# Kernel tuning notes

Measured on AMD Instinct MI355X. Metric: run time of the kernel, lower is better.

The kernel has to match this reference:

```python
import jax, jax.numpy as jnp
import numpy as np

NEG_INF = -jnp.inf


def setup_inputs() -> dict:
    key = jax.random.key(0)
    ks = jax.random.split(key, 8)
    B, C, H, W = 8, 512, 96, 96
    IC = max(1, C // 8)  # inter_channels = 64
    s = 1.0 / np.sqrt(C)
    x = jax.random.normal(ks[0], (B, C, H, W), dtype=jnp.float32)
    Wq = jax.random.normal(ks[1], (IC, C), dtype=jnp.float32) * s
    bq = jax.random.normal(ks[2], (IC,), dtype=jnp.float32) * s
    Wk = jax.random.normal(ks[3], (IC, C), dtype=jnp.float32) * s
    bk = jax.random.normal(ks[4], (IC,), dtype=jnp.float32) * s
    Wv = jax.random.normal(ks[5], (C, C), dtype=jnp.float32) * s
    bv = jax.random.normal(ks[6], (C,), dtype=jnp.float32) * s
    gamma = jnp.full((1,), 0.5, dtype=jnp.float32)  # nn.Parameter (zeros in torch; nonzero here for a non-trivial baseline)
    return {"x": x, "Wq": Wq, "bq": bq, "Wk": Wk, "bk": bk, "Wv": Wv, "bv": bv, "gamma": gamma}


def reference(x, Wq, bq, Wk, bk, Wv, bv, gamma):
    B, C, H, W = x.shape
    # 1x1 convs as channel contractions
    q = jnp.einsum('oc,bchw->bohw', Wq, x) + bq[None, :, None, None]
    k = jnp.einsum('oc,bchw->bohw', Wk, x) + bk[None, :, None, None]
    v = jnp.einsum('oc,bchw->bohw', Wv, x) + bv[None, :, None, None]
    # column (height-axis) attention logits: [B, H, W, H'] with -inf on h==h'
    e_h = jnp.einsum('bchw,bcgw->bhwg', q, k)
    eye = jnp.eye(H, dtype=bool)[:, None, :]  # [H,1,H'] broadcast over W
    e_h = jnp.where(eye[None], NEG_INF, e_h)
    # row (width-axis) attention logits: [B, H, W, W']
    e_w = jnp.einsum('bchw,bchv->bhwv', q, k)
    # joint softmax over concatenated H'+W' axis
    attn = jax.nn.softmax(jnp.concatenate([e_h, e_w], axis=-1), axis=-1)
    a_h = attn[..., :H]   # [B,H,W,H']
    a_w = attn[..., H:]   # [B,H,W,W']
    out_h = jnp.einsum('bcgw,bhwg->bchw', v, a_h)
    out_w = jnp.einsum('bchv,bhwv->bchw', v, a_w)
    return gamma[0] * (out_h + out_w) + x
```

## Files before the change

### kernel.cpp

```cpp
#include <hip/hip_runtime.h>
#include <hip/hip_bf16.h>

typedef __hip_bfloat16 bf16;
typedef unsigned short us8 __attribute__((ext_vector_type(8)));
typedef __attribute__((ext_vector_type(8))) short short8v;
typedef __attribute__((ext_vector_type(4))) float float4v;

__device__ __forceinline__ float us2f(unsigned short u){
  return __uint_as_float(((unsigned int)u) << 16);
}
__device__ __forceinline__ float b2f(bf16 v){ return __bfloat162float(v); }
__device__ __forceinline__ bf16 f2b(float v){ return __float2bfloat16(v); }
__device__ __forceinline__ unsigned short f2bu(float v){
  bf16 t = f2b(v); return *reinterpret_cast<unsigned short*>(&t);
}

#define HW 9216
#define CH 512
#define NQ 640

__global__ void k_detect(const unsigned int* __restrict__ xw, int* __restrict__ flag){
  int t = threadIdx.x;
  int cnt = 0;
  for(int i=t;i<4096;i+=256){
    unsigned e = (xw[i]>>8)&0x7F;
    if(e==0x3E||e==0x3F) cnt++;
  }
  #pragma unroll
  for(int o=32;o>0;o>>=1) cnt += __shfl_xor(cnt,o);
  __shared__ int s[4];
  if((t&63)==0) s[t>>6]=cnt;
  __syncthreads();
  if(t==0){ int tot=s[0]+s[1]+s[2]+s[3]; *flag = (tot > 1228) ? 1 : 0; }
}

__global__ void k_pack(const void* __restrict__ Wq, const void* __restrict__ Wk,
                       const void* __restrict__ Wv, const void* __restrict__ bq,
                       const void* __restrict__ bk, const void* __restrict__ bv,
                       const int* __restrict__ flag,
                       bf16* __restrict__ Wall, float* __restrict__ ball){
  bool isbf = (*flag)!=0;
  int j = blockIdx.x, t = threadIdx.x;
  const void* src = (j < 64) ? Wq : (j < 128) ? Wk : Wv;
  int row = (j < 64) ? j : (j < 128) ? (j-64) : (j-128);
  for(int c=t;c<512;c+=256){
    float v = isbf ? b2f(((const bf16*)src)[(size_t)row*512+c])
                   : ((const float*)src)[(size_t)row*512+c];
    Wall[(size_t)j*512+c] = f2b(v);
  }
  if(t==0){
    const void* bsrc = (j<64)? bq : (j<128)? bk : bv;
    ball[j] = isbf ? b2f(((const bf16*)bsrc)[row]) : ((const float*)bsrc)[row];
  }
}

__global__ __launch_bounds__(256) void k_xcvt(const void* __restrict__ x,
    const int* __restrict__ flag, bf16* __restrict__ xT){
  __shared__ float T[64][65];
  bool isbf = (*flag)!=0;
  int b = blockIdx.z, c0 = blockIdx.y*64, hw0 = blockIdx.x*64;
  int tid = threadIdx.x;
  if(isbf){
    const bf16* xb = (const bf16*)x + ((size_t)b*CH + c0)*HW + hw0;
    #pragma unroll
    for(int i=0;i<2;i++){
      int e = i*256 + tid;
      int cc = e>>3, h8 = (e&7)*8;
      us8 v = *(const us8*)(xb + (size_t)cc*HW + h8);
      #pragma unroll
      for(int j=0;j<8;j++) T[cc][h8+j] = us2f(v[j]);
    }
  } else {
    const float* xb = (const float*)x + ((size_t)b*CH + c0)*HW + hw0;
    #pragma unroll
    for(int i=0;i<4;i++){
      int e = i*256 + tid;
      int cc = e>>4, h4 = (e&15)*4;
      float4 v = *(const float4*)(xb + (size_t)cc*HW + h4);
      T[cc][h4]=v.x; T[cc][h4+1]=v.y; T[cc][h4+2]=v.z; T[cc][h4+3]=v.w;
    }
  }
  __syncthreads();
  bf16* tb = xT + ((size_t)b*HW + hw0)*512 + c0;
  #pragma unroll
  for(int i=0;i<2;i++){
    int e = i*256 + tid;
    int r = e>>3, c8 = (e&7)*8;
    us8 o;
    #pragma unroll
    for(int j=0;j<8;j++) o[j] = f2bu(T[c8+j][r]);
    *(us8*)(tb + (size_t)r*512 + c8) = o;
  }
}

__global__ __launch_bounds__(256) void k_qkv(const bf16* __restrict__ xT,
    const bf16* __restrict__ Wall, const float* __restrict__ ball,
    bf16* __restrict__ Ot){
  __shared__ ushort As[128][72];
  __shared__ ushort Bs[128][72];
  int b = blockIdx.y;
  int bx = blockIdx.x;
  int swz = (bx & 7)*45 + (bx >> 3);
  int m0 = (swz/5)*128;
  int n0 = (swz%5)*128;
  int tid = threadIdx.x, wid = tid>>6, lane = tid&63;
  int m0w = (wid>>1)*64, n0w = (wid&1)*64;
  const bf16* Ab = xT + ((size_t)b*HW + m0)*512;
  const bf16* Bb = Wall + (size_t)n0*512;
  float4v acc[4][4];
  #pragma unroll
  for(int mt=0;mt<4;mt++)
    #pragma unroll
    for(int nt=0;nt<4;nt++) acc[mt][nt] = (float4v){0.f,0.f,0.f,0.f};
  for(int k0=0;k0<512;k0+=64){
    #pragma unroll
    for(int i=0;i<4;i++){
      int s = tid + i*256;
      int row = s>>3, ko = (s&7)*8;
      us8 v = *(const us8*)(Ab + (size_t)row*512 + k0 + ko);
      *(us8*)&As[row][ko] = v;
      us8 w = *(const us8*)(Bb + (size_t)row*512 + k0 + ko);
      *(us8*)&Bs[row][ko] = w;
    }
    __syncthreads();
    #pragma unroll
    for(int kk=0;kk<64;kk+=32){
      short8v a[4], bb[4];
      #pragma unroll
      for(int mt=0;mt<4;mt++) a[mt] = *(short8v*)&As[m0w+mt*16+(lane&15)][kk+8*(lane>>4)];
      #pragma unroll
      for(int nt=0;nt<4;nt++) bb[nt] = *(short8v*)&Bs[n0w+nt*16+(lane&15)][kk+8*(lane>>4)];
      #pragma unroll
      for(int mt=0;mt<4;mt++)
        #pragma unroll
        for(int nt=0;nt<4;nt++)
          acc[mt][nt] = __builtin_amdgcn_mfma_f32_16x16x32_bf16(a[mt], bb[nt], acc[mt][nt], 0,0,0);
    }
    __syncthreads();
  }
  #pragma unroll
  for(int mt=0;mt<4;mt++){
    #pragma unroll
    for(int nt=0;nt<4;nt++){
      int nn = n0 + n0w + nt*16 + (lane&15);
      float bias = ball[nn];
      int mbase = m0 + m0w + mt*16 + (lane>>4)*4;
      #pragma unroll
      for(int r=0;r<4;r++)
        Ot[((size_t)b*HW + mbase + r)*640 + nn] = f2b(acc[mt][nt][r] + bias);
    }
  }
}

__global__ __launch_bounds__(384) void k_eh(const bf16* __restrict__ Ot,
                                            float* __restrict__ eh2){
  __shared__ ushort Qs[96][72];
  __shared__ ushort Ks[96][72];
  int b = blockIdx.y, w = blockIdx.x;
  int tid = threadIdx.x, wid = tid>>6, lane = tid&63;
  const bf16* qb = Ot + ((size_t)b*HW + w)*640;
  #pragma unroll
  for(int i=0;i<2;i++){
    int e = tid + i*384;
    int row = e>>3, ko = (e&7)*8;
    us8 q = *(const us8*)(qb + (size_t)row*96*640 + ko);
    *(us8*)&Qs[row][ko] = q;
    us8 k = *(const us8*)(qb + (size_t)row*96*640 + 64 + ko);
    *(us8*)&Ks[row][ko] = k;
  }
  __syncthreads();
  float4v acc[6];
  #pragma unroll
  for(int nt=0;nt<6;nt++) acc[nt] = (float4v){0.f,0.f,0.f,0.f};
  #pragma unroll
  for(int kt=0;kt<2;kt++){
    int kb = kt*32 + 8*(lane>>4);
    short8v a = *(short8v*)&Qs[wid*16 + (lane&15)][kb];
    #pragma unroll
    for(int nt=0;nt<6;nt++){
      short8v bb = *(short8v*)&Ks[nt*16 + (lane&15)][kb];
      acc[nt] = __builtin_amdgcn_mfma_f32_16x16x32_bf16(a, bb, acc[nt], 0,0,0);
    }
  }
  int hbase = wid*16 + (lane>>4)*4;
  #pragma unroll
  for(int nt=0;nt<6;nt++){
    int g = nt*16 + (lane&15);
    #pragma unroll
    for(int r=0;r<4;r++){
      int h = hbase + r;
      eh2[((size_t)b*HW + (size_t)h*96 + w)*96 + g] =
          (g==h) ? -INFINITY : acc[nt][r];
    }
  }
}

__global__ __launch_bounds__(384) void k_ewsm(const bf16* __restrict__ Ot,
    const float* __restrict__ eh2, bf16* __restrict__ att){
  __shared__ char smem[38400];
  ushort (*Qs)[72] = (ushort(*)[72])smem;
  ushort (*Ks)[72] = (ushort(*)[72])(smem + 13824);
  float  (*Ew)[100] = (float(*)[100])smem;
  int b = blockIdx.y, h = blockIdx.x;
  int tid = threadIdx.x, wid = tid>>6, lane = tid&63;
  const bf16* qb = Ot + ((size_t)b*HW + (size_t)h*96)*640;
  #pragma unroll
  for(int i=0;i<2;i++){
    int e = tid + i*384;
    int row = e>>3, ko = (e&7)*8;
    us8 q = *(const us8*)(qb + (size_t)row*640 + ko);
    *(us8*)&Qs[row][ko] = q;
    us8 k = *(const us8*)(qb + (size_t)row*640 + 64 + ko);
    *(us8*)&Ks[row][ko] = k;
  }
  __syncthreads();
  float4v acc[6];
  #pragma unroll
  for(int nt=0;nt<6;nt++) acc[nt] = (float4v){0.f,0.f,0.f,0.f};
  #pragma unroll
  for(int kt=0;kt<2;kt++){
    int kb = kt*32 + 8*(lane>>4);
    short8v a = *(short8v*)&Qs[wid*16 + (lane&15)][kb];
    #pragma unroll
    for(int nt=0;nt<6;nt++){
      short8v bb = *(short8v*)&Ks[nt*16 + (lane&15)][kb];
      acc[nt] = __builtin_amdgcn_mfma_f32_16x16x32_bf16(a, bb, acc[nt], 0,0,0);
    }
  }
  __syncthreads();
  int wbase = wid*16 + (lane>>4)*4;
  #pragma unroll
  for(int nt=0;nt<6;nt++){
    int v = nt*16 + (lane&15);
    #pragma unroll
    for(int r=0;r<4;r++) Ew[wbase+r][v] = acc[nt][r];
  }
  __syncthreads();
  const float* ehb = eh2 + ((size_t)b*HW + (size_t)h*96)*96;
  bf16* ab = att + ((size_t)b*HW + (size_t)h*96)*192;
  for(int r=0;r<16;r++){
    int w = wid*16 + r;
    const float* er = ehb + (size_t)w*96;
    float v0 = er[lane];
    float v1 = (lane<32) ? er[64+lane] : Ew[w][lane-32];
    float v2 = Ew[w][lane+32];
    float m = fmaxf(fmaxf(v0,v1),v2);
    #pragma unroll
    for(int o=32;o>0;o>>=1) m = fmaxf(m, __shfl_xor(m,o));
    v0=__expf(v0-m); v1=__expf(v1-m); v2=__expf(v2-m);
    float s = v0+v1+v2;
    #pragma unroll
    for(int o=32;o>0;o>>=1) s += __shfl_xor(s,o);
    float inv = 1.0f/s;
    bf16* a = ab + (size_t)w*192;
    a[lane]=f2b(v0*inv); a[lane+64]=f2b(v1*inv); a[lane+128]=f2b(v2*inv);
  }
}

__global__ __launch_bounds__(384) void k_outw(const bf16* __restrict__ Ot,
    const bf16* __restrict__ att, bf16* __restrict__ P){
  __shared__ ushort As[96][104];
  __shared__ ushort Bs[128][104];
  int b = blockIdx.y;
  int h = blockIdx.x >> 2, c0 = (blockIdx.x & 3)*128;
  int tid = threadIdx.x, wid = tid>>6, lane = tid&63;
  const bf16* ab = att + ((size_t)b*HW + (size_t)h*96)*192 + 96;
  #pragma unroll
  for(int i=0;i<3;i++){
    int s = tid + i*384;
    int row = s/12, ko = (s%12)*8;
    us8 v = *(const us8*)(ab + (size_t)row*192 + ko);
    *(us8*)&As[row][ko] = v;
  }
  const bf16* vb = Ot + ((size_t)b*HW + (size_t)h*96)*640 + 128 + c0;
  #pragma unroll
  for(int i=0;i<4;i++){
    int s = tid + i*384;
    int g = s % 96, cc = s / 96;
    us8 v = *(const us8*)(vb + (size_t)g*640 + cc*8);
    #pragma unroll
    for(int j=0;j<8;j++) Bs[cc*8+j][g] = v[j];
  }
  __syncthreads();
  float4v acc[8];
  #pragma unroll
  for(int nt=0;nt<8;nt++) acc[nt] = (float4v){0.f,0.f,0.f,0.f};
  #pragma unroll
  for(int kt=0;kt<3;kt++){
    int kb = kt*32 + 8*(lane>>4);
    short8v a = *(short8v*)&As[wid*16 + (lane&15)][kb];
    #pragma unroll
    for(int nt=0;nt<8;nt++){
      short8v bb = *(short8v*)&Bs[nt*16 + (lane&15)][kb];
      acc[nt] = __builtin_amdgcn_mfma_f32_16x16x32_bf16(a, bb, acc[nt], 0,0,0);
    }
  }
  bf16* Pb = P + ((size_t)b*HW + (size_t)h*96)*512 + c0;
  int mb = wid*16 + (lane>>4)*4;
  #pragma unroll
  for(int nt=0;nt<8;nt++){
    int n = nt*16 + (lane&15);
    #pragma unroll
    for(int r=0;r<4;r++)
      Pb[(size_t)(mb + r)*512 + n] = f2b(acc[nt][r]);
  }
}

__global__ __launch_bounds__(384) void k_outh(const bf16* __restrict__ Ot,
    const bf16* __restrict__ att, bf16* __restrict__ P){
  __shared__ ushort As[96][104];
  __shared__ ushort Bs[128][104];
  int b = blockIdx.y;
  int w = blockIdx.x >> 2, c0 = (blockIdx.x & 3)*128;
  int tid = threadIdx.x, wid = tid>>6, lane = tid&63;
  const bf16* ab = att + ((size_t)b*HW + w)*192;
  #pragma unroll
  for(int i=0;i<3;i++){
    int s = tid + i*384;
    int row = s/12, ko = (s%12)*8;
    us8 v = *(const us8*)(ab + (size_t)row*96*192 + ko);
    *(us8*)&As[row][ko] = v;
  }
  const bf16* vb = Ot + ((size_t)b*HW + w)*640 + 128 + c0;
  #pragma unroll
  for(int i=0;i<4;i++){
    int s = tid + i*384;
    int g = s % 96, cc = s / 96;
    us8 v = *(const us8*)(vb + (size_t)g*96*640 + cc*8);
    #pragma unroll
    for(int j=0;j<8;j++) Bs[cc*8+j][g] = v[j];
  }
  __syncthreads();
  float4v acc[8];
  #pragma unroll
  for(int nt=0;nt<8;nt++) acc[nt] = (float4v){0.f,0.f,0.f,0.f};
  #pragma unroll
  for(int kt=0;kt<3;kt++){
    int kb = kt*32 + 8*(lane>>4);
    short8v a = *(short8v*)&As[wid*16 + (lane&15)][kb];
    #pragma unroll
    for(int nt=0;nt<8;nt++){
      short8v bb = *(short8v*)&Bs[nt*16 + (lane&15)][kb];
      acc[nt] = __builtin_amdgcn_mfma_f32_16x16x32_bf16(a, bb, acc[nt], 0,0,0);
    }
  }
  bf16* Pb = P + ((size_t)b*HW + w)*512 + c0;
  int mb = wid*16 + (lane>>4)*4;
  #pragma unroll
  for(int nt=0;nt<8;nt++){
    int n = nt*16 + (lane&15);
    #pragma unroll
    for(int r=0;r<4;r++){
      size_t o = (size_t)(mb + r)*96*512 + n;
      Pb[o] = f2b(b2f(Pb[o]) + acc[nt][r]);
    }
  }
}

__global__ __launch_bounds__(256) void k_final(const bf16* __restrict__ P,
    const void* __restrict__ x, const void* __restrict__ gamma,
    const int* __restrict__ flag, void* __restrict__ out){
  __shared__ float T[64][65];
  bool isbf = (*flag)!=0;
  int b = blockIdx.z; int hw0 = blockIdx.x*64; int c0 = blockIdx.y*64;
  int tid = threadIdx.x;
  float g = isbf ? b2f(((const bf16*)gamma)[0]) : ((const float*)gamma)[0];
  const bf16* Pb = P + ((size_t)b*HW + hw0)*CH + c0;
  #pragma unroll
  for(int i=0;i<2;i++){
    int e = i*256 + tid;
    int r = e>>3, c8 = (e&7)*8;
    us8 v = *(const us8*)(Pb + (size_t)r*CH + c8);
    #pragma unroll
    for(int j=0;j<8;j++) T[c8+j][r] = us2f(v[j]);
  }
  __syncthreads();
  if(isbf){
    const bf16* xb = (const bf16*)x + ((size_t)b*CH + c0)*HW + hw0;
    bf16* ob = (bf16*)out + ((size_t)b*CH + c0)*HW + hw0;
    #pragma unroll
    for(int i=0;i<2;i++){
      int e = i*256 + tid;
      int cc = e>>3, h8 = (e&7)*8;
      us8 xv = *(const us8*)(xb + (size_t)cc*HW + h8);
      us8 o;
      #pragma unroll
      for(int j=0;j<8;j++) o[j] = f2bu(g*T[cc][h8+j] + us2f(xv[j]));
      *(us8*)(ob + (size_t)cc*HW + h8) = o;
    }
  } else {
    const float* xb = (const float*)x + ((size_t)b*CH + c0)*HW + hw0;
    float* ob = (float*)out + ((size_t)b*CH + c0)*HW + hw0;
    #pragma unroll
    for(int i=0;i<4;i++){
      int e = i*256 + tid;
      int cc = e>>4, h4 = (e&15)*4;
      float4 xv = *(const float4*)(xb + (size_t)cc*HW + h4);
      float4 o;
      o.x = g*T[cc][h4]   + xv.x;
      o.y = g*T[cc][h4+1] + xv.y;
      o.z = g*T[cc][h4+2] + xv.z;
      o.w = g*T[cc][h4+3] + xv.w;
      *(float4*)(ob + (size_t)cc*HW + h4) = o;
    }
  }
}

extern "C" void kernel_launch(void* const* d_in, const int* in_sizes, int n_in,
                              void* d_out, int out_size, void* d_ws, size_t ws_size,
                              hipStream_t stream){
  (void)in_sizes; (void)n_in; (void)out_size; (void)ws_size;
  const void* x     = d_in[0];
  const void* Wq    = d_in[1];
  const void* bq    = d_in[2];
  const void* Wk    = d_in[3];
  const void* bk    = d_in[4];
  const void* Wv    = d_in[5];
  const void* bv    = d_in[6];
  const void* gamma = d_in[7];
  char* ws = (char*)d_ws;

  bf16*  Wall = (bf16*)(ws + 0);
  float* ball = (float*)(ws + 655360);
  int*   flag = (int*)(ws + 657920);
  bf16*  Ot   = (bf16*)(ws + (1u<<20));
  bf16*  att  = (bf16*)(ws + 95420416ull);
  bf16*  xT   = (bf16*)(ws + 123731968ull);
  float* eh2  = (float*)(ws + 123731968ull);
  bf16*  P    = (bf16*)(ws + 123731968ull);

  hipLaunchKernelGGL(k_detect, dim3(1),       dim3(256), 0, stream,
                     (const unsigned int*)x, flag);
  hipLaunchKernelGGL(k_pack,   dim3(640),     dim3(256), 0, stream,
                     Wq, Wk, Wv, bq, bk, bv, flag, Wall, ball);
  hipLaunchKernelGGL(k_xcvt,   dim3(144,8,8), dim3(256), 0, stream, x, flag, xT);
  hipLaunchKernelGGL(k_qkv,    dim3(360,8),   dim3(256), 0, stream, xT, Wall, ball, Ot);
  hipLaunchKernelGGL(k_eh,     dim3(96,8),    dim3(384), 0, stream, Ot, eh2);
  hipLaunchKernelGGL(k_ewsm,   dim3(96,8),    dim3(384), 0, stream, Ot, eh2, att);
  hipLaunchKernelGGL(k_outw,   dim3(384,8),   dim3(384), 0, stream, Ot, att, P);
  hipLaunchKernelGGL(k_outh,   dim3(384,8),   dim3(384), 0, stream, Ot, att, P);
  hipLaunchKernelGGL(k_final,  dim3(144,8,8), dim3(256), 0, stream, P, x, gamma, flag, d_out);
}
```

Before: 311.5 us.

## Fuse width-attention output with residual epilogue and drop separate final kernel

Reorders the output stage: k_outh now writes its partial directly to P without a read-modify-write. A new k_outwf computes the width-axis attention output, adds the P partial, scales by gamma and adds x, writing the final NCHW output. It transposes the MFMA roles so each wave owns channel rows, which lets stores go straight to channel-major output. This removes one full read and write pass of P and one kernel launch. The cost is stores that are strided by HW across channels with only 16 contiguous elements per wave row, plus a fused kernel that is heavier in registers and shared memory.

```diff
diff --git a/kernel.cpp b/kernel.cpp
--- a/kernel.cpp
+++ b/kernel.cpp
@@ -257,55 +257,6 @@
   }
 }
 
-__global__ __launch_bounds__(384) void k_outw(const bf16* __restrict__ Ot,
-    const bf16* __restrict__ att, bf16* __restrict__ P){
-  __shared__ ushort As[96][104];
-  __shared__ ushort Bs[128][104];
-  int b = blockIdx.y;
-  int h = blockIdx.x >> 2, c0 = (blockIdx.x & 3)*128;
-  int tid = threadIdx.x, wid = tid>>6, lane = tid&63;
-  const bf16* ab = att + ((size_t)b*HW + (size_t)h*96)*192 + 96;
-  #pragma unroll
-  for(int i=0;i<3;i++){
-    int s = tid + i*384;
-    int row = s/12, ko = (s%12)*8;
-    us8 v = *(const us8*)(ab + (size_t)row*192 + ko);
-    *(us8*)&As[row][ko] = v;
-  }
-  const bf16* vb = Ot + ((size_t)b*HW + (size_t)h*96)*640 + 128 + c0;
-  #pragma unroll
-  for(int i=0;i<4;i++){
-    int s = tid + i*384;
-    int g = s % 96, cc = s / 96;
-    us8 v = *(const us8*)(vb + (size_t)g*640 + cc*8);
-    #pragma unroll
-    for(int j=0;j<8;j++) Bs[cc*8+j][g] = v[j];
-  }
-  __syncthreads();
-  float4v acc[8];
-  #pragma unroll
-  for(int nt=0;nt<8;nt++) acc[nt] = (float4v){0.f,0.f,0.f,0.f};
-  #pragma unroll
-  for(int kt=0;kt<3;kt++){
-    int kb = kt*32 + 8*(lane>>4);
-    short8v a = *(short8v*)&As[wid*16 + (lane&15)][kb];
-    #pragma unroll
-    for(int nt=0;nt<8;nt++){
-      short8v bb = *(short8v*)&Bs[nt*16 + (lane&15)][kb];
-      acc[nt] = __builtin_amdgcn_mfma_f32_16x16x32_bf16(a, bb, acc[nt], 0,0,0);
-    }
-  }
-  bf16* Pb = P + ((size_t)b*HW + (size_t)h*96)*512 + c0;
-  int mb = wid*16 + (lane>>4)*4;
-  #pragma unroll
-  for(int nt=0;nt<8;nt++){
-    int n = nt*16 + (lane&15);
-    #pragma unroll
-    for(int r=0;r<4;r++)
-      Pb[(size_t)(mb + r)*512 + n] = f2b(acc[nt][r]);
-  }
-}
-
 __global__ __launch_bounds__(384) void k_outh(const bf16* __restrict__ Ot,
     const bf16* __restrict__ att, bf16* __restrict__ P){
   __shared__ ushort As[96][104];
@@ -352,56 +303,71 @@
     #pragma unroll
     for(int r=0;r<4;r++){
       size_t o = (size_t)(mb + r)*96*512 + n;
-      Pb[o] = f2b(b2f(Pb[o]) + acc[nt][r]);
-    }
-  }
-}
-
-__global__ __launch_bounds__(256) void k_final(const bf16* __restrict__ P,
+      Pb[o] = f2b(acc[nt][r]);
+    }
+  }
+}
+
+__global__ __launch_bounds__(512) void k_outwf(const bf16* __restrict__ Ot,
+    const bf16* __restrict__ att, const bf16* __restrict__ P,
     const void* __restrict__ x, const void* __restrict__ gamma,
     const int* __restrict__ flag, void* __restrict__ out){
-  __shared__ float T[64][65];
+  __shared__ ushort As[96][104];
+  __shared__ ushort Bs[128][104];
   bool isbf = (*flag)!=0;
-  int b = blockIdx.z; int hw0 = blockIdx.x*64; int c0 = blockIdx.y*64;
-  int tid = threadIdx.x;
+  int b = blockIdx.y;
+  int h = blockIdx.x >> 2, c0 = (blockIdx.x & 3)*128;
+  int tid = threadIdx.x, wid = tid>>6, lane = tid&63;
   float g = isbf ? b2f(((const bf16*)gamma)[0]) : ((const float*)gamma)[0];
-  const bf16* Pb = P + ((size_t)b*HW + hw0)*CH + c0;
-  #pragma unroll
-  for(int i=0;i<2;i++){
-    int e = i*256 + tid;
-    int r = e>>3, c8 = (e&7)*8;
-    us8 v = *(const us8*)(Pb + (size_t)r*CH + c8);
-    #pragma unroll
-    for(int j=0;j<8;j++) T[c8+j][r] = us2f(v[j]);
-  }
-  __syncthreads();
-  if(isbf){
-    const bf16* xb = (const bf16*)x + ((size_t)b*CH + c0)*HW + hw0;
-    bf16* ob = (bf16*)out + ((size_t)b*CH + c0)*HW + hw0;
-    #pragma unroll
-    for(int i=0;i<2;i++){
-      int e = i*256 + tid;
-      int cc = e>>3, h8 = (e&7)*8;
-      us8 xv = *(const us8*)(xb + (size_t)cc*HW + h8);
-      us8 o;
-      #pragma unroll
-      for(int j=0;j<8;j++) o[j] = f2bu(g*T[cc][h8+j] + us2f(xv[j]));
-      *(us8*)(ob + (size_t)cc*HW + h8) = o;
-    }
-  } else {
-    const float* xb = (const float*)x + ((size_t)b*CH + c0)*HW + hw0;
-    float* ob = (float*)out + ((size_t)b*CH + c0)*HW + hw0;
-    #pragma unroll
-    for(int i=0;i<4;i++){
-      int e = i*256 + tid;
-      int cc = e>>4, h4 = (e&15)*4;
-      float4 xv = *(const float4*)(xb + (size_t)cc*HW + h4);
-      float4 o;
-      o.x = g*T[cc][h4]   + xv.x;
-      o.y = g*T[cc][h4+1] + xv.y;
-      o.z = g*T[cc][h4+2] + xv.z;
-      o.w = g*T[cc][h4+3] + xv.w;
-      *(float4*)(ob + (size_t)cc*HW + h4) = o;
+  const bf16* ab = att + ((size_t)b*HW + (size_t)h*96)*192 + 96;
+  #pragma unroll
+  for(int i=0;i<3;i++){
+    int s = tid + i*512;
+    if(s < 1152){
+      int row = s/12, ko = (s%12)*8;
+      us8 v = *(const us8*)(ab + (size_t)row*192 + ko);
+      *(us8*)&As[row][ko] = v;
+    }
+  }
+  const bf16* vb = Ot + ((size_t)b*HW + (size_t)h*96)*640 + 128 + c0;
+  #pragma unroll
+  for(int i=0;i<3;i++){
+    int s = tid + i*512;
+    int gg = s % 96, cc = s / 96;
+    us8 v = *(const us8*)(vb + (size_t)gg*640 + cc*8);
+    #pragma unroll
+    for(int j=0;j<8;j++) Bs[cc*8+j][gg] = v[j];
+  }
+  __syncthreads();
+  float4v acc[6];
+  #pragma unroll
+  for(int nt=0;nt<6;nt++) acc[nt] = (float4v){0.f,0.f,0.f,0.f};
+  #pragma unroll
+  for(int kt=0;kt<3;kt++){
+    int kb = kt*32 + 8*(lane>>4);
+    short8v a = *(short8v*)&Bs[wid*16 + (lane&15)][kb];
+    #pragma unroll
+    for(int nt=0;nt<6;nt++){
+      short8v bb = *(short8v*)&As[nt*16 + (lane&15)][kb];
+      acc[nt] = __builtin_amdgcn_mfma_f32_16x16x32_bf16(a, bb, acc[nt], 0,0,0);
+    }
+  }
+  int clb = wid*16 + (lane>>4)*4;
+  const bf16* Pb = P + ((size_t)b*HW + (size_t)h*96)*512 + c0;
+  size_t xbase = ((size_t)b*CH + c0)*HW + (size_t)h*96;
+  #pragma unroll
+  for(int nt=0;nt<6;nt++){
+    int w = nt*16 + (lane&15);
+    #pragma unroll
+    for(int r=0;r<4;r++){
+      int c = clb + r;
+      float sum = acc[nt][r] + b2f(Pb[(size_t)w*512 + c]);
+      size_t o = xbase + (size_t)c*HW + w;
+      if(isbf){
+        ((bf16*)out)[o] = f2b(g*sum + b2f(((const bf16*)x)[o]));
+      } else {
+        ((float*)out)[o] = g*sum + ((const float*)x)[o];
+      }
     }
   }
 }
@@ -437,7 +403,7 @@
   hipLaunchKernelGGL(k_qkv,    dim3(360,8),   dim3(256), 0, stream, xT, Wall, ball, Ot);
   hipLaunchKernelGGL(k_eh,     dim3(96,8),    dim3(384), 0, stream, Ot, eh2);
   hipLaunchKernelGGL(k_ewsm,   dim3(96,8),    dim3(384), 0, stream, Ot, eh2, att);
-  hipLaunchKernelGGL(k_outw,   dim3(384,8),   dim3(384), 0, stream, Ot, att, P);
   hipLaunchKernelGGL(k_outh,   dim3(384,8),   dim3(384), 0, stream, Ot, att, P);
-  hipLaunchKernelGGL(k_final,  dim3(144,8,8), dim3(256), 0, stream, P, x, gamma, flag, d_out);
-}
+  hipLaunchKernelGGL(k_outwf,  dim3(384,8),   dim3(512), 0, stream,
+                     Ot, att, P, x, gamma, flag, d_out);
+}
```

New measurement: 363.2 us. 1.17x slower.
